# Kernel optimization log

Hardware: AMD Instinct MI355X
Metric: run time of the kernel (lower is better)

The kernel has to match this reference:

```python
import jax, jax.numpy as jnp
import numpy as np

B, R, C, COILS, SEGS, POL, PAD = 4, 256, 256, 32, 4, 2, 20


def _fft2c(x):
    # centered 2D FFT over axes (1,2) with 1/sqrt(R*C) norm (matches fft2c_coil_tf_buda)
    scale = 1.0 / np.sqrt(x.shape[1] * x.shape[2]).astype(np.float32)
    x = jnp.fft.fftshift(x, axes=(1, 2))
    x = jnp.fft.fft2(x, axes=(1, 2))
    return jnp.fft.fftshift(x, axes=(1, 2)) * scale


def _ifft2c(x):
    # centered 2D IFFT over axes (1,2) with sqrt(R*C) norm (matches ifft2c_coil_tf_buda)
    scale = np.sqrt(x.shape[1] * x.shape[2]).astype(np.float32)
    x = jnp.fft.ifftshift(x, axes=(1, 2))
    x = jnp.fft.ifft2(x, axes=(1, 2))
    return jnp.fft.ifftshift(x, axes=(1, 2)) * scale


def _center_crop(x, h, w):
    oh = (x.shape[1] - h) // 2
    ow = (x.shape[2] - w) // 2
    return x[:, oh:oh + h, ow:ow + w]


def _center_pad(x, h, w):
    ph = h - x.shape[1]
    pw = w - x.shape[2]
    pads = [(0, 0), (ph // 2, ph - ph // 2), (pw // 2, pw - pw // 2), (0, 0)]
    return jnp.pad(x, pads)


def setup_inputs() -> dict:
    key = jax.random.key(0)
    ks = jax.random.split(key, 7)
    return {
        "x_re": jax.random.normal(ks[0], (B, R + PAD, C + PAD, POL), jnp.float32),
        "x_im": jax.random.normal(ks[1], (B, R + PAD, C + PAD, POL), jnp.float32),
        "csm_re": jax.random.normal(ks[2], (B, R, C, COILS), jnp.float32),
        "csm_im": jax.random.normal(ks[3], (B, R, C, COILS), jnp.float32),
        "wmap_re": jax.random.normal(ks[4], (B, R, C, POL, SEGS), jnp.float32),
        "wmap_im": jax.random.normal(ks[5], (B, R, C, POL, SEGS), jnp.float32),
        "mask": jax.random.randint(ks[6], (B, R, C, POL, SEGS), 0, 2).astype(jnp.float32),
        "num_rows": R, "num_cols": C, "num_coils": COILS,
        "num_segs": SEGS, "num_polarities": POL,
    }


def reference(x_re, x_im, csm_re, csm_im, wmap_re, wmap_im, mask,
              num_rows, num_cols, num_coils, num_segs, num_polarities):
    x = (x_re + 1j * x_im).astype(jnp.complex64)
    csm = (csm_re + 1j * csm_im).astype(jnp.complex64)      # [B,R,C,coil]
    wmap = (wmap_re + 1j * wmap_im).astype(jnp.complex64)   # [B,R,C,pol,seg]

    # ---- forward model A ----
    img = _center_crop(x, num_rows, num_cols)                # [B,R,C,pol]
    # broadcast instead of tf.tile: [B,R,C,coil,pol,seg]
    tmp_i = (img[:, :, :, None, :, None]
             * wmap[:, :, :, None, :, :]
             * csm[:, :, :, :, None, None])
    tmp_k = _fft2c(tmp_i)
    kspace = jnp.sum(tmp_k * mask[:, :, :, None, :, :], axis=-1)  # [B,R,C,coil,pol]

    # ---- adjoint model A^H ----
    tk = kspace[..., None] * mask[:, :, :, None, :, :]       # [B,R,C,coil,pol,seg]
    ti = _ifft2c(tk)
    ti = ti * jnp.conj(wmap)[:, :, :, None, :, :] * jnp.conj(csm)[:, :, :, :, None, None]
    out = jnp.sum(ti, axis=(3, 5))                           # sum coils and segments -> [B,R,C,pol]

    out = _center_pad(out, num_rows + PAD, num_rows + PAD)   # tf pads both dims with num_rows+20
    return jnp.stack([out.real, out.imag], axis=-1)          # [B,R+20,R+20,pol,2]
```

## Files before the change

### kernel.cpp

```cpp
#include <hip/hip_runtime.h>
#include <hip/hip_fp16.h>

#define NB 4
#define NR 256
#define NC 256
#define NCOIL 32
#define NSEG 4
#define NPOL 2
#define OD 276
#define OFF 10
#define NCC 16

typedef float2 c32;

__device__ __forceinline__ c32 cmul(c32 a, c32 b){
  return make_float2(a.x*b.x - a.y*b.y, a.x*b.y + a.y*b.x);
}
__device__ __forceinline__ c32 cmulj(c32 a, c32 b){
  return make_float2(a.x*b.x + a.y*b.y, a.y*b.x - a.x*b.y);
}
__device__ __forceinline__ int pd(int a){ return a + (a >> 4); }
__device__ __forceinline__ void wsync(){ __builtin_amdgcn_wave_barrier(); }

struct TW { c32 t1[4]; c32 t2[4]; c32 t3[4]; };
__device__ __forceinline__ void mk_tw(int u, TW& T){
  #pragma unroll
  for (int s = 0; s < 4; ++s){
    int e = u & ~((1 << (2*s)) - 1);
    float a = -0.0245436926061703f * (float)e;
    float sn, cs; sincosf(a, &sn, &cs);
    c32 w1 = make_float2(cs, sn);
    T.t1[s] = w1;
    T.t2[s] = cmul(w1, w1);
    T.t3[s] = cmul(T.t2[s], w1);
  }
}

template<int DIR>
__device__ __forceinline__ void fft256(c32* x, c32* b0, c32* b1,
                                       const TW& T, int u){
  #pragma unroll
  for (int s = 0; s < 4; ++s){
    const int m = 1 << (2*s);
    c32 a0, a1, a2, a3;
    if (s == 0){ a0 = x[0]; a1 = x[1]; a2 = x[2]; a3 = x[3]; }
    else {
      const c32* src = ((s & 1) ? b0 : b1);
      a0 = src[pd(u)]; a1 = src[pd(u+64)]; a2 = src[pd(u+128)]; a3 = src[pd(u+192)];
    }
    c32 s0 = make_float2(a0.x+a2.x, a0.y+a2.y);
    c32 d0 = make_float2(a0.x-a2.x, a0.y-a2.y);
    c32 s1 = make_float2(a1.x+a3.x, a1.y+a3.y);
    c32 d1 = make_float2(a1.x-a3.x, a1.y-a3.y);
    c32 X0 = make_float2(s0.x+s1.x, s0.y+s1.y);
    c32 X2 = make_float2(s0.x-s1.x, s0.y-s1.y);
    c32 X1, X3;
    if (DIR > 0){
      X1 = make_float2(d0.x + d1.y, d0.y - d1.x);
      X3 = make_float2(d0.x - d1.y, d0.y + d1.x);
    } else {
      X1 = make_float2(d0.x - d1.y, d0.y + d1.x);
      X3 = make_float2(d0.x + d1.y, d0.y - d1.x);
    }
    c32 w1 = T.t1[s], w2 = T.t2[s], w3 = T.t3[s];
    if (DIR < 0){ w1.y = -w1.y; w2.y = -w2.y; w3.y = -w3.y; }
    X1 = cmul(X1, w1); X2 = cmul(X2, w2); X3 = cmul(X3, w3);
    if (s == 3){
      x[0] = X0; x[1] = X1; x[2] = X2; x[3] = X3;
    } else {
      c32* dst = ((s & 1) ? b1 : b0);
      int j = u >> (2*s);
      int k = u & (m-1);
      int base = k + 4*m*j;
      dst[pd(base)]      = X0;
      dst[pd(base+m)]    = X1;
      dst[pd(base+2*m)]  = X2;
      dst[pd(base+3*m)]  = X3;
    }
    wsync();
  }
}

__global__ __launch_bounds__(256) void zero_kernel(float* __restrict__ out, int n){
  int i = blockIdx.x*256 + threadIdx.x;
  if (i < n) out[i] = 0.0f;
}

__global__ __launch_bounds__(256) void pack_common_kernel(
    const float* __restrict__ x_re, const float* __restrict__ x_im,
    const float* __restrict__ wm_re, const float* __restrict__ wm_im,
    const float* __restrict__ mask,
    c32* __restrict__ img_t, c32* __restrict__ w_t, float* __restrict__ m_t)
{
  int r = blockIdx.x & (NR-1);
  int bl = blockIdx.x >> 8;
  int c = threadIdx.x;
  const size_t PL = (size_t)NR*NC;
  float sc = (((r + c) & 1) ? -1.0f : 1.0f) * (1.0f/256.0f);
  size_t xrow = (((size_t)bl*OD) + (r+OFF))*OD + (c+OFF);
  #pragma unroll
  for (int pol = 0; pol < NPOL; ++pol){
    size_t xi = xrow*NPOL + pol;
    img_t[((size_t)(bl*NPOL+pol))*PL + (size_t)r*NC + c] =
        make_float2(x_re[xi]*sc, x_im[xi]*sc);
  }
  size_t wbase = (((size_t)bl*NR + r)*NC + c)*(NPOL*NSEG);
  const float4* wre4 = (const float4*)&wm_re[wbase];
  const float4* wim4 = (const float4*)&wm_im[wbase];
  const float4* mk4  = (const float4*)&mask[wbase];
  #pragma unroll
  for (int pol = 0; pol < NPOL; ++pol){
    float4 re = wre4[pol], im = wim4[pol], mk = mk4[pol];
    float rr[4] = {re.x, re.y, re.z, re.w};
    float ii[4] = {im.x, im.y, im.z, im.w};
    float mm[4] = {mk.x, mk.y, mk.z, mk.w};
    #pragma unroll
    for (int seg = 0; seg < NSEG; ++seg){
      int ps = bl*(NPOL*NSEG) + pol*NSEG + seg;
      w_t[(size_t)ps*PL + (size_t)r*NC + c] = make_float2(rr[seg], ii[seg]);
      m_t[(size_t)ps*PL + (size_t)c*NR + r] = mm[seg];
    }
  }
}

__global__ __launch_bounds__(256) void pack_csm_kernel(
    int b,
    const float* __restrict__ csm_re, const float* __restrict__ csm_im,
    c32* __restrict__ c_t)
{
  int r = blockIdx.x;
  int c = threadIdx.x;
  const size_t PL = (size_t)NR*NC;
  size_t base = (((size_t)b*NR + r)*NC + c)*NCOIL;
  c32* cp = c_t + (size_t)r*NC + c;
  for (int cl = 0; cl < NCOIL; cl += 4){
    float4 re = *(const float4*)&csm_re[base + cl];
    float4 im = *(const float4*)&csm_im[base + cl];
    cp[(size_t)(cl+0)*PL] = make_float2(re.x, im.x);
    cp[(size_t)(cl+1)*PL] = make_float2(re.y, im.y);
    cp[(size_t)(cl+2)*PL] = make_float2(re.z, im.z);
    cp[(size_t)(cl+3)*PL] = make_float2(re.w, im.w);
  }
}

__global__ __launch_bounds__(256) void stageA_kernel(
    const c32* __restrict__ img_t, const c32* __restrict__ w_t,
    const c32* __restrict__ c_t, __half2* __restrict__ T1)
{
  __shared__ c32 fbuf[4][2][272];
  __shared__ __half2 tile[NC*17];
  int tid = threadIdx.x;
  int u = tid & 63, w = tid >> 6;
  TW T; mk_tw(u, T);
  int bid = blockIdx.x;
  int p  = bid >> 4;
  int rt = bid & 15;
  int seg = p & 3, pol = (p>>2) & 1, cl = p >> 3;

  for (int ri = 0; ri < 4; ++ri){
    int rl = w*4 + ri;
    int r = rt*16 + rl;
    const c32* ir = img_t + ((size_t)pol*NR + r)*NC;
    const c32* wr = w_t  + ((size_t)(pol*NSEG+seg)*NR + r)*NC;
    const c32* cr = c_t  + ((size_t)cl*NR + r)*NC;
    c32 x[4];
    #pragma unroll
    for (int i = 0; i < 4; ++i){
      int c = u + 64*i;
      x[i] = cmul(cmul(ir[c], wr[c]), cr[c]);
    }
    fft256<1>(x, fbuf[w][0], fbuf[w][1], T, u);
    #pragma unroll
    for (int t = 0; t < 4; ++t){
      int c = u + 64*t;
      tile[c*17 + rl] = __floats2half2_rn(x[t].x, x[t].y);
    }
  }
  __syncthreads();
  __half2* tp = T1 + (size_t)p*(NR*NC);
  int r0 = rt*16;
  #pragma unroll
  for (int cb = 0; cb < 16; ++cb){
    int cc = w*64 + cb*4 + (u >> 4);
    int rl = u & 15;
    tp[cc*NR + r0 + rl] = tile[cc*17 + rl];
  }
}

__global__ __launch_bounds__(256) void stageB_kernel(
    const __half2* __restrict__ T1, const float* __restrict__ m_t,
    __half2* __restrict__ T2)
{
  __shared__ c32 fbuf[4][2][272];
  __shared__ __half2 tile[16][256];
  int tid = threadIdx.x, u = tid & 63, w = tid >> 6;
  TW T; mk_tw(u, T);
  int bid = blockIdx.x;
  int ct = bid & 15;
  int g  = bid >> 4;
  int pol = g & 1;
  int c0 = ct*16;
  const size_t PL = (size_t)NR*NC;

  c32 K[4][4];
  #pragma unroll
  for (int j = 0; j < 4; ++j)
    #pragma unroll
    for (int t = 0; t < 4; ++t) K[j][t] = make_float2(0.f, 0.f);

  #pragma unroll
  for (int j = 0; j < 4; ++j){
    int col = c0 + w*4 + j;
    #pragma unroll 1
    for (int seg = 0; seg < NSEG; ++seg){
      const __half2* tp = T1 + ((size_t)(g*NSEG+seg))*PL + (size_t)col*NR;
      const float*  mp = m_t + ((size_t)(pol*NSEG+seg))*PL + (size_t)col*NR;
      c32 x[4];
      float mv[4];
      #pragma unroll
      for (int i = 0; i < 4; ++i){
        x[i]  = __half22float2(tp[u + 64*i]);
        mv[i] = mp[u + 64*i];
      }
      fft256<1>(x, fbuf[w][0], fbuf[w][1], T, u);
      #pragma unroll
      for (int t = 0; t < 4; ++t){
        K[j][t].x += mv[t]*x[t].x;
        K[j][t].y += mv[t]*x[t].y;
      }
    }
  }
  #pragma unroll 1
  for (int seg = 0; seg < NSEG; ++seg){
    #pragma unroll
    for (int j = 0; j < 4; ++j){
      int col = c0 + w*4 + j;
      const float* mp = m_t + ((size_t)(pol*NSEG+seg))*PL + (size_t)col*NR;
      c32 x[4];
      #pragma unroll
      for (int t = 0; t < 4; ++t){
        float mv = mp[u + 64*t];
        x[t] = make_float2(K[j][t].x*mv, K[j][t].y*mv);
      }
      fft256<-1>(x, fbuf[w][0], fbuf[w][1], T, u);
      #pragma unroll
      for (int t = 0; t < 4; ++t)
        tile[w*4+j][u + 64*t] = __floats2half2_rn(x[t].x*(1.0f/256.0f),
                                                  x[t].y*(1.0f/256.0f));
    }
    __syncthreads();
    {
      int r = tid;
      unsigned pk[16];
      #pragma unroll
      for (int k = 0; k < 16; ++k){
        __half2 h = tile[k][r];
        pk[k] = *(unsigned*)&h;
      }
      uint4* dst = (uint4*)(T2 + ((size_t)(g*NSEG+seg))*PL + (size_t)r*NC + c0);
      dst[0] = make_uint4(pk[0],  pk[1],  pk[2],  pk[3]);
      dst[1] = make_uint4(pk[4],  pk[5],  pk[6],  pk[7]);
      dst[2] = make_uint4(pk[8],  pk[9],  pk[10], pk[11]);
      dst[3] = make_uint4(pk[12], pk[13], pk[14], pk[15]);
    }
    __syncthreads();
  }
}

__global__ __launch_bounds__(256) void stageC_part_kernel(
    const __half2* __restrict__ T2, const c32* __restrict__ w_t,
    const c32* __restrict__ c_t, __half2* __restrict__ part, int ch0)
{
  __shared__ c32 fbuf[4][2][272];
  int tid = threadIdx.x, u = tid & 63, w = tid >> 6;
  TW T; mk_tw(u, T);
  int bid = blockIdx.x;
  int rq = bid & 63, pol = (bid>>6) & 1, ch = bid >> 7;
  int r = rq*4 + w;
  const size_t PL = (size_t)NR*NC;

  c32 acc[4];
  #pragma unroll
  for (int t = 0; t < 4; ++t) acc[t] = make_float2(0.f, 0.f);

  __half2 v[4];
  {
    const __half2* rp = T2 + ((size_t)((ch*2*NPOL+pol)*NSEG))*PL + (size_t)r*NC;
    #pragma unroll
    for (int i = 0; i < 4; ++i) v[i] = rp[u + 64*i];
  }
  #pragma unroll 1
  for (int pl = 0; pl < 2*NSEG; ++pl){
    int cl = ch*2 + (pl>>2), seg = pl & 3;
    c32 x[4];
    #pragma unroll
    for (int i = 0; i < 4; ++i) x[i] = __half22float2(v[i]);
    if (pl < 2*NSEG-1){
      int cl2 = ch*2 + ((pl+1)>>2), seg2 = (pl+1) & 3;
      const __half2* rp = T2 + ((size_t)((cl2*NPOL+pol)*NSEG+seg2))*PL + (size_t)r*NC;
      #pragma unroll
      for (int i = 0; i < 4; ++i) v[i] = rp[u + 64*i];
    }
    const c32* wr = w_t + ((size_t)(pol*NSEG+seg)*NR + r)*NC;
    const c32* cr = c_t + ((size_t)cl*NR + r)*NC;
    c32 wv[4], cv[4];
    #pragma unroll
    for (int t = 0; t < 4; ++t){ wv[t] = wr[u + 64*t]; cv[t] = cr[u + 64*t]; }
    fft256<-1>(x, fbuf[w][0], fbuf[w][1], T, u);
    #pragma unroll
    for (int t = 0; t < 4; ++t){
      c32 vv = cmulj(x[t], wv[t]);
      vv = cmulj(vv, cv[t]);
      acc[t].x += vv.x;
      acc[t].y += vv.y;
    }
  }
  __half2* pp = part + ((size_t)((ch0+ch)*NPOL+pol))*PL + (size_t)r*NC;
  #pragma unroll
  for (int t = 0; t < 4; ++t)
    pp[u + 64*t] = __floats2half2_rn(acc[t].x, acc[t].y);
}

__global__ __launch_bounds__(256) void reduceC_kernel(
    int b, const __half2* __restrict__ part, float* __restrict__ out)
{
  int r = blockIdx.x, c = threadIdx.x;
  const size_t PL = (size_t)NR*NC;
  float2 s[NPOL];
  #pragma unroll
  for (int pol = 0; pol < NPOL; ++pol) s[pol] = make_float2(0.f, 0.f);
  #pragma unroll 4
  for (int ch = 0; ch < NCC; ++ch){
    #pragma unroll
    for (int pol = 0; pol < NPOL; ++pol){
      float2 f = __half22float2(part[((size_t)(ch*NPOL+pol))*PL + (size_t)r*NC + c]);
      s[pol].x += f.x; s[pol].y += f.y;
    }
  }
  float sgn = ((r + c) & 1) ? -1.0f : 1.0f;
  float4 o = make_float4(sgn*s[0].x, sgn*s[0].y, sgn*s[1].x, sgn*s[1].y);
  size_t oidx = (((size_t)b*OD + (r+OFF))*OD + (c+OFF));
  ((float4*)out)[oidx] = o;
}

extern "C" void kernel_launch(void* const* d_in, const int* in_sizes, int n_in,
                              void* d_out, int out_size, void* d_ws, size_t ws_size,
                              hipStream_t stream)
{
  (void)in_sizes; (void)n_in;
  const float* x_re   = (const float*)d_in[0];
  const float* x_im   = (const float*)d_in[1];
  const float* csm_re = (const float*)d_in[2];
  const float* csm_im = (const float*)d_in[3];
  const float* wm_re  = (const float*)d_in[4];
  const float* wm_im  = (const float*)d_in[5];
  const float* mask   = (const float*)d_in[6];

  const size_t PL = (size_t)NR*NC;
  const size_t imgB1 = (size_t)NPOL*PL*sizeof(c32);
  const size_t wB1   = (size_t)NPOL*NSEG*PL*sizeof(c32);
  const size_t mB1   = (size_t)NPOL*NSEG*PL*sizeof(float);
  const size_t csmB1 = (size_t)NCOIL*PL*sizeof(c32);
  const size_t partB = (size_t)NCC*NPOL*PL*4;
  const size_t coilB = (size_t)NPOL*NSEG*PL*4;

  const size_t fixed = NB*(imgB1 + wB1 + mB1) + csmB1 + partB;

  int CH = 32;
  while (CH > 4){
    if (fixed + (size_t)CH*2*coilB <= ws_size) break;
    CH >>= 1;
  }

  char* ws = (char*)d_ws;
  c32* img_t = (c32*)ws;
  c32* w_t   = (c32*)(ws + NB*imgB1);
  float* m_t = (float*)(ws + NB*(imgB1 + wB1));
  c32* c_t   = (c32*)(ws + NB*(imgB1 + wB1 + mB1));
  __half2* part = (__half2*)(ws + NB*(imgB1 + wB1 + mB1) + csmB1);
  __half2* T1 = (__half2*)(ws + fixed);
  __half2* T2 = (__half2*)(ws + fixed + (size_t)CH*coilB);

  float* out = (float*)d_out;
  zero_kernel<<<(out_size + 255)/256, 256, 0, stream>>>(out, out_size);

  pack_common_kernel<<<NB*NR, 256, 0, stream>>>(x_re, x_im, wm_re, wm_im,
                                                mask, img_t, w_t, m_t);
  for (int b = 0; b < NB; ++b){
    c32* img_b = img_t + (size_t)b*NPOL*PL;
    c32* w_b   = w_t   + (size_t)b*NPOL*NSEG*PL;
    float* m_b = m_t   + (size_t)b*NPOL*NSEG*PL;
    pack_csm_kernel<<<NR, 256, 0, stream>>>(b, csm_re, csm_im, c_t);
    for (int c0 = 0; c0 < NCOIL; c0 += CH){
      c32* c_b = c_t + (size_t)c0*PL;
      stageA_kernel<<<CH*NPOL*NSEG*16, 256, 0, stream>>>(img_b, w_b, c_b, T1);
      stageB_kernel<<<CH*NPOL*16, 256, 0, stream>>>(T1, m_b, T2);
      stageC_part_kernel<<<(CH/2)*NPOL*64, 256, 0, stream>>>(T2, w_b, c_b,
                                                             part, c0/2);
    }
    reduceC_kernel<<<NR, 256, 0, stream>>>(b, part, out);
  }
}
```

Measured before the change: 607.7 us.

## Replace radix-4 LDS FFT with register radix-16 two-pass FFT-256

Replaces the 4-stage radix-4 FFT, which makes three LDS round trips per transform with one 64-lane wave per row, with a 16x16 decomposition. Each group of 16 lanes owns one row and keeps 16 values in registers, with a single XOR-swizzled LDS transpose between two register DFT16 passes. Each wave now handles four rows at once, so stageC launches a quarter as many blocks and each thread processes 16 elements. This cuts LDS traffic and barriers, but raises register pressure and may reduce occupancy and the grid size of stageC.

```diff
diff --git a/kernel.cpp b/kernel.cpp
--- a/kernel.cpp
+++ b/kernel.cpp
@@ -19,66 +19,80 @@
 __device__ __forceinline__ c32 cmulj(c32 a, c32 b){
   return make_float2(a.x*b.x + a.y*b.y, a.y*b.x - a.x*b.y);
 }
-__device__ __forceinline__ int pd(int a){ return a + (a >> 4); }
+__device__ __forceinline__ c32 cmulc(c32 a, float br, float bi){
+  return make_float2(a.x*br - a.y*bi, a.x*bi + a.y*br);
+}
 __device__ __forceinline__ void wsync(){ __builtin_amdgcn_wave_barrier(); }
 
-struct TW { c32 t1[4]; c32 t2[4]; c32 t3[4]; };
-__device__ __forceinline__ void mk_tw(int u, TW& T){
-  #pragma unroll
-  for (int s = 0; s < 4; ++s){
-    int e = u & ~((1 << (2*s)) - 1);
-    float a = -0.0245436926061703f * (float)e;
-    float sn, cs; sincosf(a, &sn, &cs);
-    c32 w1 = make_float2(cs, sn);
-    T.t1[s] = w1;
-    T.t2[s] = cmul(w1, w1);
-    T.t3[s] = cmul(T.t2[s], w1);
-  }
-}
+#define C16A 0.9238795325112867f
+#define S16A 0.3826834323650898f
+#define RSQ2 0.7071067811865476f
 
 template<int DIR>
-__device__ __forceinline__ void fft256(c32* x, c32* b0, c32* b1,
-                                       const TW& T, int u){
-  #pragma unroll
-  for (int s = 0; s < 4; ++s){
-    const int m = 1 << (2*s);
-    c32 a0, a1, a2, a3;
-    if (s == 0){ a0 = x[0]; a1 = x[1]; a2 = x[2]; a3 = x[3]; }
-    else {
-      const c32* src = ((s & 1) ? b0 : b1);
-      a0 = src[pd(u)]; a1 = src[pd(u+64)]; a2 = src[pd(u+128)]; a3 = src[pd(u+192)];
-    }
-    c32 s0 = make_float2(a0.x+a2.x, a0.y+a2.y);
-    c32 d0 = make_float2(a0.x-a2.x, a0.y-a2.y);
-    c32 s1 = make_float2(a1.x+a3.x, a1.y+a3.y);
-    c32 d1 = make_float2(a1.x-a3.x, a1.y-a3.y);
-    c32 X0 = make_float2(s0.x+s1.x, s0.y+s1.y);
-    c32 X2 = make_float2(s0.x-s1.x, s0.y-s1.y);
-    c32 X1, X3;
-    if (DIR > 0){
-      X1 = make_float2(d0.x + d1.y, d0.y - d1.x);
-      X3 = make_float2(d0.x - d1.y, d0.y + d1.x);
-    } else {
-      X1 = make_float2(d0.x - d1.y, d0.y + d1.x);
-      X3 = make_float2(d0.x + d1.y, d0.y - d1.x);
-    }
-    c32 w1 = T.t1[s], w2 = T.t2[s], w3 = T.t3[s];
-    if (DIR < 0){ w1.y = -w1.y; w2.y = -w2.y; w3.y = -w3.y; }
-    X1 = cmul(X1, w1); X2 = cmul(X2, w2); X3 = cmul(X3, w3);
-    if (s == 3){
-      x[0] = X0; x[1] = X1; x[2] = X2; x[3] = X3;
-    } else {
-      c32* dst = ((s & 1) ? b1 : b0);
-      int j = u >> (2*s);
-      int k = u & (m-1);
-      int base = k + 4*m*j;
-      dst[pd(base)]      = X0;
-      dst[pd(base+m)]    = X1;
-      dst[pd(base+2*m)]  = X2;
-      dst[pd(base+3*m)]  = X3;
-    }
-    wsync();
-  }
+__device__ __forceinline__ void r4(c32 a0, c32 a1, c32 a2, c32 a3,
+                                   c32& o0, c32& o1, c32& o2, c32& o3){
+  c32 s0 = make_float2(a0.x+a2.x, a0.y+a2.y);
+  c32 d0 = make_float2(a0.x-a2.x, a0.y-a2.y);
+  c32 s1 = make_float2(a1.x+a3.x, a1.y+a3.y);
+  c32 d1 = make_float2(a1.x-a3.x, a1.y-a3.y);
+  o0 = make_float2(s0.x+s1.x, s0.y+s1.y);
+  o2 = make_float2(s0.x-s1.x, s0.y-s1.y);
+  if (DIR > 0){
+    o1 = make_float2(d0.x + d1.y, d0.y - d1.x);
+    o3 = make_float2(d0.x - d1.y, d0.y + d1.x);
+  } else {
+    o1 = make_float2(d0.x - d1.y, d0.y + d1.x);
+    o3 = make_float2(d0.x + d1.y, d0.y - d1.x);
+  }
+}
+
+template<int DIR>
+__device__ __forceinline__ void dft16(c32* y){
+  const float sg = (DIR > 0) ? -1.0f : 1.0f;
+  c32 g[16];
+  #pragma unroll
+  for (int b = 0; b < 4; ++b)
+    r4<DIR>(y[b], y[b+4], y[b+8], y[b+12], g[b], g[4+b], g[8+b], g[12+b]);
+  g[5]  = cmulc(g[5],  C16A,  sg*S16A);
+  g[6]  = cmulc(g[6],  RSQ2,  sg*RSQ2);
+  g[7]  = cmulc(g[7],  S16A,  sg*C16A);
+  g[9]  = cmulc(g[9],  RSQ2,  sg*RSQ2);
+  g[10] = cmulc(g[10], 0.0f,  sg);
+  g[11] = cmulc(g[11], -RSQ2, sg*RSQ2);
+  g[13] = cmulc(g[13], S16A,  sg*C16A);
+  g[14] = cmulc(g[14], -RSQ2, sg*RSQ2);
+  g[15] = cmulc(g[15], -C16A, -sg*S16A);
+  #pragma unroll
+  for (int c = 0; c < 4; ++c)
+    r4<DIR>(g[4*c], g[4*c+1], g[4*c+2], g[4*c+3],
+            y[c], y[c+4], y[c+8], y[c+12]);
+}
+
+__device__ __forceinline__ void mk_tw16(int l, c32* tw){
+  float sn, cs;
+  sincosf(-0.0245436926061703f * (float)l, &sn, &cs);
+  c32 base = make_float2(cs, sn);
+  tw[0] = make_float2(1.0f, 0.0f);
+  #pragma unroll
+  for (int r = 1; r < 16; ++r) tw[r] = cmul(tw[r-1], base);
+}
+
+template<int DIR>
+__device__ __forceinline__ void fft256g(c32* y, const c32* tw, c32* sc,
+                                        int l, int g){
+  dft16<DIR>(y);
+  #pragma unroll
+  for (int r = 1; r < 16; ++r)
+    y[r] = (DIR > 0) ? cmul(y[r], tw[r]) : cmulj(y[r], tw[r]);
+  #pragma unroll
+  for (int r = 0; r < 16; ++r)
+    sc[((r*4 + g) << 4) + (l ^ r)] = y[r];
+  wsync();
+  #pragma unroll
+  for (int j = 0; j < 16; ++j)
+    y[j] = sc[((l*4 + g) << 4) + (j ^ l)];
+  wsync();
+  dft16<DIR>(y);
 }
 
 __global__ __launch_bounds__(256) void zero_kernel(float* __restrict__ out, int n){
@@ -147,43 +161,41 @@
     const c32* __restrict__ img_t, const c32* __restrict__ w_t,
     const c32* __restrict__ c_t, __half2* __restrict__ T1)
 {
-  __shared__ c32 fbuf[4][2][272];
-  __shared__ __half2 tile[NC*17];
+  __shared__ c32 fsc[4][1024];
+  __shared__ __half2 tile[NC*20];
   int tid = threadIdx.x;
-  int u = tid & 63, w = tid >> 6;
-  TW T; mk_tw(u, T);
+  int l = tid & 15, g = (tid >> 4) & 3, w = tid >> 6;
+  c32 tw[16]; mk_tw16(l, tw);
   int bid = blockIdx.x;
   int p  = bid >> 4;
   int rt = bid & 15;
   int seg = p & 3, pol = (p>>2) & 1, cl = p >> 3;
-
-  for (int ri = 0; ri < 4; ++ri){
-    int rl = w*4 + ri;
-    int r = rt*16 + rl;
-    const c32* ir = img_t + ((size_t)pol*NR + r)*NC;
-    const c32* wr = w_t  + ((size_t)(pol*NSEG+seg)*NR + r)*NC;
-    const c32* cr = c_t  + ((size_t)cl*NR + r)*NC;
-    c32 x[4];
-    #pragma unroll
-    for (int i = 0; i < 4; ++i){
-      int c = u + 64*i;
-      x[i] = cmul(cmul(ir[c], wr[c]), cr[c]);
-    }
-    fft256<1>(x, fbuf[w][0], fbuf[w][1], T, u);
-    #pragma unroll
-    for (int t = 0; t < 4; ++t){
-      int c = u + 64*t;
-      tile[c*17 + rl] = __floats2half2_rn(x[t].x, x[t].y);
-    }
-  }
+  int r = rt*16 + 4*w + g;
+
+  const c32* ir = img_t + ((size_t)pol*NR + r)*NC;
+  const c32* wr = w_t  + ((size_t)(pol*NSEG+seg)*NR + r)*NC;
+  const c32* cr = c_t  + ((size_t)cl*NR + r)*NC;
+  c32 y[16];
+  #pragma unroll
+  for (int i = 0; i < 16; ++i){
+    int c = 16*i + l;
+    y[i] = cmul(cmul(ir[c], wr[c]), cr[c]);
+  }
+  fft256g<1>(y, tw, fsc[w], l, g);
+  int rl = 4*w + g;
+  #pragma unroll
+  for (int j = 0; j < 16; ++j)
+    tile[(l + 16*j)*20 + rl] = __floats2half2_rn(y[j].x, y[j].y);
   __syncthreads();
-  __half2* tp = T1 + (size_t)p*(NR*NC);
-  int r0 = rt*16;
-  #pragma unroll
-  for (int cb = 0; cb < 16; ++cb){
-    int cc = w*64 + cb*4 + (u >> 4);
-    int rl = u & 15;
-    tp[cc*NR + r0 + rl] = tile[cc*17 + rl];
+  __half2* tp = T1 + (size_t)p*(NR*NC) + (size_t)tid*NR + rt*16;
+  const __half2* trow = tile + tid*20;
+  #pragma unroll
+  for (int k = 0; k < 4; ++k){
+    __half2 h0 = trow[4*k+0], h1 = trow[4*k+1];
+    __half2 h2 = trow[4*k+2], h3 = trow[4*k+3];
+    uint4 q = make_uint4(*(unsigned*)&h0, *(unsigned*)&h1,
+                         *(unsigned*)&h2, *(unsigned*)&h3);
+    *(uint4*)(tp + 4*k) = q;
   }
 }
 
@@ -191,73 +203,61 @@
     const __half2* __restrict__ T1, const float* __restrict__ m_t,
     __half2* __restrict__ T2)
 {
-  __shared__ c32 fbuf[4][2][272];
-  __shared__ __half2 tile[16][256];
-  int tid = threadIdx.x, u = tid & 63, w = tid >> 6;
-  TW T; mk_tw(u, T);
+  __shared__ c32 fsc[4][1024];
+  __shared__ __half2 tile[16*272];
+  int tid = threadIdx.x;
+  int l = tid & 15, g = (tid >> 4) & 3, w = tid >> 6;
+  c32 tw[16]; mk_tw16(l, tw);
   int bid = blockIdx.x;
   int ct = bid & 15;
-  int g  = bid >> 4;
-  int pol = g & 1;
-  int c0 = ct*16;
-  const size_t PL = (size_t)NR*NC;
-
-  c32 K[4][4];
-  #pragma unroll
-  for (int j = 0; j < 4; ++j)
-    #pragma unroll
-    for (int t = 0; t < 4; ++t) K[j][t] = make_float2(0.f, 0.f);
-
-  #pragma unroll
-  for (int j = 0; j < 4; ++j){
-    int col = c0 + w*4 + j;
-    #pragma unroll 1
-    for (int seg = 0; seg < NSEG; ++seg){
-      const __half2* tp = T1 + ((size_t)(g*NSEG+seg))*PL + (size_t)col*NR;
-      const float*  mp = m_t + ((size_t)(pol*NSEG+seg))*PL + (size_t)col*NR;
-      c32 x[4];
-      float mv[4];
-      #pragma unroll
-      for (int i = 0; i < 4; ++i){
-        x[i]  = __half22float2(tp[u + 64*i]);
-        mv[i] = mp[u + 64*i];
-      }
-      fft256<1>(x, fbuf[w][0], fbuf[w][1], T, u);
-      #pragma unroll
-      for (int t = 0; t < 4; ++t){
-        K[j][t].x += mv[t]*x[t].x;
-        K[j][t].y += mv[t]*x[t].y;
-      }
-    }
-  }
+  int gp = bid >> 4;
+  int pol = gp & 1;
+  int col = ct*16 + 4*w + g;
+  const size_t PL = (size_t)NR*NC;
+
+  c32 K[16];
+  #pragma unroll
+  for (int j = 0; j < 16; ++j) K[j] = make_float2(0.f, 0.f);
+
   #pragma unroll 1
   for (int seg = 0; seg < NSEG; ++seg){
-    #pragma unroll
-    for (int j = 0; j < 4; ++j){
-      int col = c0 + w*4 + j;
-      const float* mp = m_t + ((size_t)(pol*NSEG+seg))*PL + (size_t)col*NR;
-      c32 x[4];
-      #pragma unroll
-      for (int t = 0; t < 4; ++t){
-        float mv = mp[u + 64*t];
-        x[t] = make_float2(K[j][t].x*mv, K[j][t].y*mv);
-      }
-      fft256<-1>(x, fbuf[w][0], fbuf[w][1], T, u);
-      #pragma unroll
-      for (int t = 0; t < 4; ++t)
-        tile[w*4+j][u + 64*t] = __floats2half2_rn(x[t].x*(1.0f/256.0f),
-                                                  x[t].y*(1.0f/256.0f));
-    }
+    const __half2* tp = T1 + ((size_t)(gp*NSEG+seg))*PL + (size_t)col*NR;
+    const float*  mp = m_t + ((size_t)(pol*NSEG+seg)*NC + col)*NR;
+    c32 y[16];
+    #pragma unroll
+    for (int i = 0; i < 16; ++i) y[i] = __half22float2(tp[16*i + l]);
+    fft256g<1>(y, tw, fsc[w], l, g);
+    #pragma unroll
+    for (int j = 0; j < 16; ++j){
+      float mv = mp[l + 16*j];
+      K[j].x += mv*y[j].x;
+      K[j].y += mv*y[j].y;
+    }
+  }
+  #pragma unroll 1
+  for (int seg = 0; seg < NSEG; ++seg){
+    const float* mp = m_t + ((size_t)(pol*NSEG+seg)*NC + col)*NR;
+    c32 y[16];
+    #pragma unroll
+    for (int j = 0; j < 16; ++j){
+      float mv = mp[l + 16*j];
+      y[j] = make_float2(K[j].x*mv, K[j].y*mv);
+    }
+    fft256g<-1>(y, tw, fsc[w], l, g);
+    #pragma unroll
+    for (int i = 0; i < 16; ++i)
+      tile[(4*w+g)*272 + 16*i + l] = __floats2half2_rn(y[i].x*(1.0f/256.0f),
+                                                       y[i].y*(1.0f/256.0f));
     __syncthreads();
     {
-      int r = tid;
       unsigned pk[16];
       #pragma unroll
       for (int k = 0; k < 16; ++k){
-        __half2 h = tile[k][r];
+        __half2 h = tile[k*272 + tid];
         pk[k] = *(unsigned*)&h;
       }
-      uint4* dst = (uint4*)(T2 + ((size_t)(g*NSEG+seg))*PL + (size_t)r*NC + c0);
+      uint4* dst = (uint4*)(T2 + ((size_t)(gp*NSEG+seg))*PL
+                            + (size_t)tid*NC + ct*16);
       dst[0] = make_uint4(pk[0],  pk[1],  pk[2],  pk[3]);
       dst[1] = make_uint4(pk[4],  pk[5],  pk[6],  pk[7]);
       dst[2] = make_uint4(pk[8],  pk[9],  pk[10], pk[11]);
@@ -271,54 +271,43 @@
     const __half2* __restrict__ T2, const c32* __restrict__ w_t,
     const c32* __restrict__ c_t, __half2* __restrict__ part, int ch0)
 {
-  __shared__ c32 fbuf[4][2][272];
-  int tid = threadIdx.x, u = tid & 63, w = tid >> 6;
-  TW T; mk_tw(u, T);
+  __shared__ c32 fsc[4][1024];
+  int tid = threadIdx.x;
+  int l = tid & 15, g = (tid >> 4) & 3, w = tid >> 6;
+  c32 tw[16]; mk_tw16(l, tw);
   int bid = blockIdx.x;
-  int rq = bid & 63, pol = (bid>>6) & 1, ch = bid >> 7;
-  int r = rq*4 + w;
-  const size_t PL = (size_t)NR*NC;
-
-  c32 acc[4];
-  #pragma unroll
-  for (int t = 0; t < 4; ++t) acc[t] = make_float2(0.f, 0.f);
-
-  __half2 v[4];
-  {
-    const __half2* rp = T2 + ((size_t)((ch*2*NPOL+pol)*NSEG))*PL + (size_t)r*NC;
-    #pragma unroll
-    for (int i = 0; i < 4; ++i) v[i] = rp[u + 64*i];
-  }
+  int rt = bid & 15, pol = (bid>>4) & 1, ch = bid >> 5;
+  int r = rt*16 + 4*w + g;
+  const size_t PL = (size_t)NR*NC;
+
+  c32 acc[16];
+  #pragma unroll
+  for (int i = 0; i < 16; ++i) acc[i] = make_float2(0.f, 0.f);
+
   #pragma unroll 1
   for (int pl = 0; pl < 2*NSEG; ++pl){
     int cl = ch*2 + (pl>>2), seg = pl & 3;
-    c32 x[4];
-    #pragma unroll
-    for (int i = 0; i < 4; ++i) x[i] = __half22float2(v[i]);
-    if (pl < 2*NSEG-1){
-      int cl2 = ch*2 + ((pl+1)>>2), seg2 = (pl+1) & 3;
-      const __half2* rp = T2 + ((size_t)((cl2*NPOL+pol)*NSEG+seg2))*PL + (size_t)r*NC;
-      #pragma unroll
-      for (int i = 0; i < 4; ++i) v[i] = rp[u + 64*i];
-    }
+    const __half2* rp = T2 + ((size_t)((cl*NPOL+pol)*NSEG+seg))*PL
+                        + (size_t)r*NC;
+    c32 y[16];
+    #pragma unroll
+    for (int j = 0; j < 16; ++j) y[j] = __half22float2(rp[l + 16*j]);
+    fft256g<-1>(y, tw, fsc[w], l, g);
     const c32* wr = w_t + ((size_t)(pol*NSEG+seg)*NR + r)*NC;
     const c32* cr = c_t + ((size_t)cl*NR + r)*NC;
-    c32 wv[4], cv[4];
-    #pragma unroll
-    for (int t = 0; t < 4; ++t){ wv[t] = wr[u + 64*t]; cv[t] = cr[u + 64*t]; }
-    fft256<-1>(x, fbuf[w][0], fbuf[w][1], T, u);
-    #pragma unroll
-    for (int t = 0; t < 4; ++t){
-      c32 vv = cmulj(x[t], wv[t]);
-      vv = cmulj(vv, cv[t]);
-      acc[t].x += vv.x;
-      acc[t].y += vv.y;
+    #pragma unroll
+    for (int i = 0; i < 16; ++i){
+      int c = 16*i + l;
+      c32 vv = cmulj(y[i], wr[c]);
+      vv = cmulj(vv, cr[c]);
+      acc[i].x += vv.x;
+      acc[i].y += vv.y;
     }
   }
   __half2* pp = part + ((size_t)((ch0+ch)*NPOL+pol))*PL + (size_t)r*NC;
   #pragma unroll
-  for (int t = 0; t < 4; ++t)
-    pp[u + 64*t] = __floats2half2_rn(acc[t].x, acc[t].y);
+  for (int i = 0; i < 16; ++i)
+    pp[16*i + l] = __floats2half2_rn(acc[i].x, acc[i].y);
 }
 
 __global__ __launch_bounds__(256) void reduceC_kernel(
@@ -395,7 +384,7 @@
       c32* c_b = c_t + (size_t)c0*PL;
       stageA_kernel<<<CH*NPOL*NSEG*16, 256, 0, stream>>>(img_b, w_b, c_b, T1);
       stageB_kernel<<<CH*NPOL*16, 256, 0, stream>>>(T1, m_b, T2);
-      stageC_part_kernel<<<(CH/2)*NPOL*64, 256, 0, stream>>>(T2, w_b, c_b,
+      stageC_part_kernel<<<(CH/2)*NPOL*16, 256, 0, stream>>>(T2, w_b, c_b,
                                                              part, c0/2);
     }
     reduceC_kernel<<<NR, 256, 0, stream>>>(b, part, out);
```

Result: faster. 584.5 us (-3.8%).
